# Performance work log

Hardware: AMD Instinct MI355X
Metric: run time of the kernel (lower is better)

## Reference

```python
import jax, jax.numpy as jnp
import numpy as np

P = 50000  # dimension of parameter vector p
H = W = 28  # hardcoded image size in the original module
CARD = 50


def setup_inputs() -> dict:
    key = jax.random.key(0)
    k1, k2, k3, k4, k5 = jax.random.split(key, 5)
    p = jax.random.normal(k1, (P,), dtype=jnp.float32)
    I = jax.random.normal(k2, (H * W, P), dtype=jnp.float32) / np.sqrt(P)
    J = jax.random.normal(k3, (H * W, P), dtype=jnp.float32) / np.sqrt(P)
    # Cubical persistence indices: opaque CPU output, stop_gradient'ed in the
    # original -> modeled as int32 constants. Shape [2*card, D] with D=2.
    inds1 = jax.random.randint(k4, (2 * CARD, 2), 0, H, dtype=jnp.int32)
    inds2 = jax.random.randint(k5, (2 * CARD, 2), 0, H, dtype=jnp.int32)
    return {"p": p, "I": I, "J": J, "inds1": inds1, "inds2": inds2}


def reference(p, I, J, inds1, inds2):
    # Xp = reshape(tensordot(I, p, 1), [28, 28])
    Xp = (I @ p).reshape(H, W)
    Yp = (J @ p).reshape(H, W)
    # dgm = reshape(gather_nd(Xp, inds), [-1, 2]) -> [card, 2] diagram
    dgm1 = Xp[inds1[:, 0], inds1[:, 1]].reshape(-1, 2)
    dgm2 = Yp[inds2[:, 0], inds2[:, 1]].reshape(-1, 2)
    return (dgm1, dgm2)
```

## Files before the change

kernel.cpp:

```cpp
#include <hip/hip_runtime.h>


#define P_DIM 50000
#define NV    (P_DIM / 4)
#define NGATH 100
#define NOUT  200
#define SPLIT 8
#define CHUNK ((NV + SPLIT - 1) / SPLIT)

__global__ __launch_bounds__(256) void gather_dot_partial(
    const float* __restrict__ p,
    const float* __restrict__ I,
    const float* __restrict__ J,
    const int*   __restrict__ inds1,
    const int*   __restrict__ inds2,
    float*       __restrict__ partials)
{
    const int b = blockIdx.x;
    const int o = b / SPLIT;
    const int s = b % SPLIT;

    const float* mat;
    const int*   ind;
    int k;
    if (o < NGATH) { mat = I; ind = inds1; k = o; }
    else           { mat = J; ind = inds2; k = o - NGATH; }

    const int r = ind[2 * k];
    const int c = ind[2 * k + 1];
    const size_t flat = (size_t)(r * 28 + c);

    const float4* __restrict__ row = (const float4*)(mat + flat * (size_t)P_DIM);
    const float4* __restrict__ p4  = (const float4*)p;

    const int start = s * CHUNK;
    const int end   = (start + CHUNK < NV) ? (start + CHUNK) : NV;

    float s0 = 0.f, s1 = 0.f;
    int i = start + (int)threadIdx.x;
    for (; i + 256 < end; i += 512) {
        float4 a0 = row[i];
        float4 p0 = p4[i];
        float4 a1 = row[i + 256];
        float4 p1 = p4[i + 256];
        s0 += a0.x * p0.x + a0.y * p0.y + a0.z * p0.z + a0.w * p0.w;
        s1 += a1.x * p1.x + a1.y * p1.y + a1.z * p1.z + a1.w * p1.w;
    }
    if (i < end) {
        float4 a0 = row[i];
        float4 p0 = p4[i];
        s0 += a0.x * p0.x + a0.y * p0.y + a0.z * p0.z + a0.w * p0.w;
    }
    float sum = s0 + s1;

    #pragma unroll
    for (int off = 32; off > 0; off >>= 1)
        sum += __shfl_down(sum, off, 64);

    __shared__ float smem[4];
    const int lane = threadIdx.x & 63;
    const int wave = threadIdx.x >> 6;
    if (lane == 0) smem[wave] = sum;
    __syncthreads();

    if (threadIdx.x == 0) {
        partials[o * SPLIT + s] = smem[0] + smem[1] + smem[2] + smem[3];
    }
}

__global__ void reduce_partials(const float* __restrict__ partials,
                                float* __restrict__ out)
{
    const int o = blockIdx.x * blockDim.x + threadIdx.x;
    if (o < NOUT) {
        float t = 0.f;
        #pragma unroll
        for (int s = 0; s < SPLIT; ++s) t += partials[o * SPLIT + s];
        out[o] = t;
    }
}

extern "C" void kernel_launch(void* const* d_in, const int* in_sizes, int n_in,
                              void* d_out, int out_size, void* d_ws, size_t ws_size,
                              hipStream_t stream) {
    const float* p     = (const float*)d_in[0];
    const float* I     = (const float*)d_in[1];
    const float* J     = (const float*)d_in[2];
    const int*   inds1 = (const int*)d_in[3];
    const int*   inds2 = (const int*)d_in[4];
    float* out      = (float*)d_out;
    float* partials = (float*)d_ws;

    gather_dot_partial<<<NOUT * SPLIT, 256, 0, stream>>>(p, I, J, inds1, inds2, partials);
    reduce_partials<<<1, 256, 0, stream>>>(partials, out);
}
```

Measured before the change: 259.1 us.

## Fuse split-K partial dot and reduction into one 1024-thread block per output

Replaces the two-kernel scheme (8 split blocks per output writing partials, then a reduce kernel) with one kernel launching 200 blocks of 1024 threads, each computing a full gathered-row dot product with 4-way unrolled float4 loads. It removes the second launch and the partials round trip. In exchange only 200 blocks run, which may underfill the GPU's 256 CUs and lower memory-level parallelism for this bandwidth-bound gather.

```diff
diff --git a/kernel.cpp b/kernel.cpp
--- a/kernel.cpp
+++ b/kernel.cpp
@@ -5,20 +5,17 @@
 #define NV    (P_DIM / 4)
 #define NGATH 100
 #define NOUT  200
-#define SPLIT 8
-#define CHUNK ((NV + SPLIT - 1) / SPLIT)
+#define BLOCK 1024
 
-__global__ __launch_bounds__(256) void gather_dot_partial(
+__global__ __launch_bounds__(BLOCK) void gather_dot_fused(
     const float* __restrict__ p,
     const float* __restrict__ I,
     const float* __restrict__ J,
     const int*   __restrict__ inds1,
     const int*   __restrict__ inds2,
-    float*       __restrict__ partials)
+    float*       __restrict__ out)
 {
-    const int b = blockIdx.x;
-    const int o = b / SPLIT;
-    const int s = b % SPLIT;
+    const int o = blockIdx.x;
 
     const float* mat;
     const int*   ind;
@@ -33,50 +30,41 @@
     const float4* __restrict__ row = (const float4*)(mat + flat * (size_t)P_DIM);
     const float4* __restrict__ p4  = (const float4*)p;
 
-    const int start = s * CHUNK;
-    const int end   = (start + CHUNK < NV) ? (start + CHUNK) : NV;
-
-    float s0 = 0.f, s1 = 0.f;
-    int i = start + (int)threadIdx.x;
-    for (; i + 256 < end; i += 512) {
-        float4 a0 = row[i];
-        float4 p0 = p4[i];
-        float4 a1 = row[i + 256];
-        float4 p1 = p4[i + 256];
-        s0 += a0.x * p0.x + a0.y * p0.y + a0.z * p0.z + a0.w * p0.w;
-        s1 += a1.x * p1.x + a1.y * p1.y + a1.z * p1.z + a1.w * p1.w;
+    float s0 = 0.f, s1 = 0.f, s2 = 0.f, s3 = 0.f;
+    int i = (int)threadIdx.x;
+    for (; i + 3 * BLOCK < NV; i += 4 * BLOCK) {
+        float4 a0 = row[i];             float4 b0 = p4[i];
+        float4 a1 = row[i + BLOCK];     float4 b1 = p4[i + BLOCK];
+        float4 a2 = row[i + 2 * BLOCK]; float4 b2 = p4[i + 2 * BLOCK];
+        float4 a3 = row[i + 3 * BLOCK]; float4 b3 = p4[i + 3 * BLOCK];
+        s0 += a0.x * b0.x + a0.y * b0.y + a0.z * b0.z + a0.w * b0.w;
+        s1 += a1.x * b1.x + a1.y * b1.y + a1.z * b1.z + a1.w * b1.w;
+        s2 += a2.x * b2.x + a2.y * b2.y + a2.z * b2.z + a2.w * b2.w;
+        s3 += a3.x * b3.x + a3.y * b3.y + a3.z * b3.z + a3.w * b3.w;
     }
-    if (i < end) {
-        float4 a0 = row[i];
-        float4 p0 = p4[i];
-        s0 += a0.x * p0.x + a0.y * p0.y + a0.z * p0.z + a0.w * p0.w;
+    for (; i < NV; i += BLOCK) {
+        float4 a = row[i];
+        float4 b = p4[i];
+        s0 += a.x * b.x + a.y * b.y + a.z * b.z + a.w * b.w;
     }
-    float sum = s0 + s1;
+    float sum = (s0 + s1) + (s2 + s3);
 
     #pragma unroll
     for (int off = 32; off > 0; off >>= 1)
         sum += __shfl_down(sum, off, 64);
 
-    __shared__ float smem[4];
+    __shared__ float smem[BLOCK / 64];
     const int lane = threadIdx.x & 63;
     const int wave = threadIdx.x >> 6;
     if (lane == 0) smem[wave] = sum;
     __syncthreads();
 
-    if (threadIdx.x == 0) {
-        partials[o * SPLIT + s] = smem[0] + smem[1] + smem[2] + smem[3];
-    }
-}
-
-__global__ void reduce_partials(const float* __restrict__ partials,
-                                float* __restrict__ out)
-{
-    const int o = blockIdx.x * blockDim.x + threadIdx.x;
-    if (o < NOUT) {
-        float t = 0.f;
+    if (threadIdx.x < 64) {
+        float v = (threadIdx.x < BLOCK / 64) ? smem[threadIdx.x] : 0.f;
         #pragma unroll
-        for (int s = 0; s < SPLIT; ++s) t += partials[o * SPLIT + s];
-        out[o] = t;
+        for (int off = 8; off > 0; off >>= 1)
+            v += __shfl_down(v, off, 64);
+        if (threadIdx.x == 0) out[o] = v;
     }
 }
 
@@ -88,9 +76,7 @@
     const float* J     = (const float*)d_in[2];
     const int*   inds1 = (const int*)d_in[3];
     const int*   inds2 = (const int*)d_in[4];
-    float* out      = (float*)d_out;
-    float* partials = (float*)d_ws;
+    float* out = (float*)d_out;
 
-    gather_dot_partial<<<NOUT * SPLIT, 256, 0, stream>>>(p, I, J, inds1, inds2, partials);
-    reduce_partials<<<1, 256, 0, stream>>>(partials, out);
+    gather_dot_fused<<<NOUT, BLOCK, 0, stream>>>(p, I, J, inds1, inds2, out);
 }
```

New measurement: 260.5 us. About the same (+0.5%).
